# Optimization experiments

Hardware: AMD Instinct MI355X
Metric: run time of the kernel (lower is better)

The kernel has to match this reference:

```python
import jax, jax.numpy as jnp
from jax import lax
import numpy as np

B, T, F = 64, 128, 16
H = 512
S = 2  # num_seg; SEG_DICT['2'] = [8, 6], seg_cumsum = [2, 10, 16]


def timestep_embedding(t, dim, max_period=10000.0):
    half = dim // 2
    freqs = jnp.exp(-jnp.log(max_period) * jnp.arange(half, dtype=jnp.float32) / half)
    args = t[:, None] * freqs  # [N, half]
    return jnp.concatenate([jnp.cos(args), jnp.sin(args)], axis=-1)  # [N, dim]


def setup_inputs() -> dict:
    key = jax.random.key(0)
    ks = jax.random.split(key, 16)
    sc = lambda *sh: 1.0 / np.sqrt(sh[-1])
    inp = {
        'x': jax.random.normal(ks[0], (B, T, F), dtype=jnp.float32),
        'lengths': jax.random.randint(ks[1], (B,), 1, T + 1),
        'h0': jax.random.uniform(ks[2], (B, H), dtype=jnp.float32),
        'c0': jax.random.uniform(ks[3], (B, H), dtype=jnp.float32),
        'W_is0': jax.random.normal(ks[4], (H, 8), dtype=jnp.float32) * sc(8),
        'b_is0': jax.random.normal(ks[5], (H,), dtype=jnp.float32) * 0.01,
        'W_is1': jax.random.normal(ks[6], (H, 6), dtype=jnp.float32) * sc(6),
        'b_is1': jax.random.normal(ks[7], (H,), dtype=jnp.float32) * 0.01,
        'W_ih': jax.random.normal(ks[8], (4 * H, 3 * H), dtype=jnp.float32) * sc(3 * H),
        'W_hh': jax.random.normal(ks[9], (4 * H, H), dtype=jnp.float32) * sc(H),
        'b_ih': jax.random.normal(ks[10], (4 * H,), dtype=jnp.float32) * 0.01,
        'b_hh': jax.random.normal(ks[11], (4 * H,), dtype=jnp.float32) * 0.01,
        'W_o': jax.random.normal(ks[12], (F - 2, S * H), dtype=jnp.float32) * sc(S * H),
        'b_o': jax.random.normal(ks[13], (F - 2,), dtype=jnp.float32) * 0.01,
    }
    return inp


def reference(x, lengths, h0, c0, W_is0, b_is0, W_is1, b_is1,
              W_ih, W_hh, b_ih, b_hh, W_o, b_o):
    b, t, f = x.shape
    h = h0.shape[1]
    xf = x.reshape(-1, f)  # [B*T, F]

    # timestep embeddings from the two time columns (learning_type='diff')
    tc = timestep_embedding(xf[:, 0], h)
    tp = timestep_embedding(xf[:, 1], h)
    t_emb = jnp.concatenate([tc, tp], axis=-1)  # [B*T, 2H]

    # per-segment input linears (segments = cols 2:10 and 10:16)
    e0 = xf[:, 2:10] @ W_is0.T + b_is0
    e1 = xf[:, 10:16] @ W_is1.T + b_is1
    e0 = jnp.concatenate([e0, t_emb], axis=-1)[:, None, :]  # [B*T, 1, 3H]
    e1 = jnp.concatenate([e1, t_emb], axis=-1)[:, None, :]
    # faithful to torch: concat on dim=1 then reshape(batch, num_seg, seq_len, -1)
    embs = jnp.concatenate([e0, e1], axis=1).reshape(b, S, t, 3 * h)

    def cell(carry, xt):
        hh, cc = carry
        gates = xt @ W_ih.T + b_ih + hh @ W_hh.T + b_hh
        i, fg, g, o = jnp.split(gates, 4, axis=-1)  # torch LSTMCell order i,f,g,o
        cc = jax.nn.sigmoid(fg) * cc + jax.nn.sigmoid(i) * jnp.tanh(g)
        hh = jax.nn.sigmoid(o) * jnp.tanh(cc)
        return (hh, cc), hh

    hs = []
    for s in range(S):  # shared cell weights across segments (same nn.LSTMCell object)
        xs = jnp.swapaxes(embs[:, s], 0, 1)  # [T, B, 3H]
        _, h_seq = lax.scan(cell, (h0, c0), xs)  # [T, B, H]
        hs.append(jnp.swapaxes(h_seq, 0, 1))  # [B, T, H]
    hidden_states = jnp.stack(hs, axis=-2)  # [B, T, S, H]; dropout rate 0 -> identity

    idx = lengths - 1  # final valid timestep per sequence
    hfin = hidden_states[jnp.arange(b), idx].reshape(b, S * h)  # [B, S*H]
    out = jax.nn.sigmoid(hfin @ W_o.T + b_o)  # mlp_o: Linear + Sigmoid
    return out
```

## Files before the change

### kernel.cpp

```cpp
#include <hip/hip_runtime.h>
#include <hip/hip_bf16.h>
#include <stdint.h>


typedef __attribute__((ext_vector_type(8))) short bf16x8_t;
typedef __attribute__((ext_vector_type(4))) float f32x4_t;

#define SENT 0xAAAAAAAAu

#define OFF_G      0u
#define OFF_TEMB   33554432u
#define OFF_HH     50331648u
#define OFF_WHH    67239936u
#define OFF_WMID   69337088u
#define OFF_WC0    73531392u
#define OFF_WC1    73596928u
#define OFF_BC     73662464u
#define OFF_HFIN   73678848u

__device__ __forceinline__ float bf2f(uint16_t u){
  union { uint32_t i; float f; } v; v.i = ((uint32_t)u) << 16; return v.f;
}
__device__ __forceinline__ uint16_t f2b(float f){
  union { float f; uint32_t i; } v; v.f = f;
  uint32_t r = v.i + 0x7fffu + ((v.i >> 16) & 1u);
  return (uint16_t)(r >> 16);
}
__device__ __forceinline__ float sigm(float x){ return 1.0f/(1.0f + __expf(-x)); }
__device__ __forceinline__ float tanh_(float x){
  float xc = fminf(fmaxf(x, -15.f), 15.f);
  float t = __expf(2.f*xc);
  return (t - 1.f)/(t + 1.f);
}

__global__ void prep1(const float* __restrict__ W_ih, const float* __restrict__ W_hh,
                      const float* __restrict__ W_is0, const float* __restrict__ b_is0,
                      const float* __restrict__ W_is1, const float* __restrict__ b_is1,
                      const float* __restrict__ b_ih, const float* __restrict__ b_hh,
                      uint16_t* __restrict__ whh_b, uint16_t* __restrict__ wmid_b,
                      float* __restrict__ wc0, float* __restrict__ wc1, float* __restrict__ bc){
  const int n = blockIdx.x;
  const int tid = threadIdx.x;
  __shared__ float wrow[512];
  wrow[tid]       = W_ih[(size_t)n*1536 + tid];
  wrow[tid + 256] = W_ih[(size_t)n*1536 + 256 + tid];
  for (int j = tid; j < 1024; j += 256)
    wmid_b[(size_t)n*1024 + j] = f2b(W_ih[(size_t)n*1536 + 512 + j]);
  for (int k = tid; k < 512; k += 256)
    whh_b[(size_t)n*512 + k] = f2b(W_hh[(size_t)n*512 + k]);
  __syncthreads();
  if (tid < 8){
    float s = 0.f;
    for (int k = 0; k < 512; ++k) s += wrow[k]*W_is0[k*8 + tid];
    wc0[n*8 + tid] = s;
  } else if (tid < 16){
    int c = tid - 8;
    float s = 0.f;
    if (c < 6){ for (int k = 0; k < 512; ++k) s += wrow[k]*W_is1[k*6 + c]; }
    wc1[n*8 + c] = s;
  } else if (tid == 16){
    float s = b_ih[n] + b_hh[n];
    for (int k = 0; k < 512; ++k) s += wrow[k]*b_is0[k];
    bc[n] = s;
  } else if (tid == 17){
    float s = b_ih[n] + b_hh[n];
    for (int k = 0; k < 512; ++k) s += wrow[k]*b_is1[k];
    bc[2048 + n] = s;
  }
}

__global__ void prep2(const float* __restrict__ h0, uint16_t* __restrict__ h_hist){
  int i = blockIdx.x*256 + threadIdx.x;
  uint32_t* hh = (uint32_t*)h_hist;
  if (i < 32768){
    int rw = i >> 8, k = (i & 255)*2;
    uint32_t lo = f2b(h0[(size_t)(rw & 63)*512 + k]);
    uint32_t hi = f2b(h0[(size_t)(rw & 63)*512 + k + 1]);
    uint32_t w = lo | (hi << 16);
    if (w == SENT) w ^= 1u;
    hh[i] = w;
  } else if (i < 4227072){
    hh[i] = SENT;
  }
}

__global__ void tembk(const float* __restrict__ x, uint16_t* __restrict__ temb){
  const int rid = blockIdx.x;
  const int k = threadIdx.x;
  float x0 = x[(size_t)rid*16 + 0], x1 = x[(size_t)rid*16 + 1];
  float f = __expf((float)k * (-9.210340371976184f/256.f));
  float a0 = x0*f, a1 = x1*f;
  size_t base = (size_t)rid*1024;
  temb[base + k]        = f2b(__cosf(a0));
  temb[base + 256 + k]  = f2b(__sinf(a0));
  temb[base + 512 + k]  = f2b(__cosf(a1));
  temb[base + 768 + k]  = f2b(__sinf(a1));
}

__launch_bounds__(256)
__global__ void gemmB(const uint16_t* __restrict__ temb, const uint16_t* __restrict__ wmid,
                      uint16_t* __restrict__ G){
  __shared__ __align__(16) uint16_t Al[128][72];
  __shared__ __align__(16) uint16_t Bl[128][72];
  const int tid = threadIdx.x;
  const int m0 = blockIdx.x*128, n0 = blockIdx.y*128;
  const int w = tid >> 6, lane = tid & 63;
  const int q = lane >> 4, ln = lane & 15;
  const int wm = w >> 1, wn = w & 1;
  const int srow = tid >> 1, shalf = tid & 1;

  f32x4_t acc[4][4];
  #pragma unroll
  for (int a = 0; a < 4; ++a)
    #pragma unroll
    for (int b = 0; b < 4; ++b) acc[a][b] = (f32x4_t){0.f,0.f,0.f,0.f};

  for (int kb = 0; kb < 16; ++kb){
    const uint4* ga = (const uint4*)(temb + (size_t)(m0 + srow)*1024 + kb*64 + shalf*32);
    const uint4* gb = (const uint4*)(wmid + (size_t)(n0 + srow)*1024 + kb*64 + shalf*32);
    uint4 va[4], vb[4];
    #pragma unroll
    for (int i = 0; i < 4; ++i){ va[i] = ga[i]; vb[i] = gb[i]; }
    #pragma unroll
    for (int i = 0; i < 4; ++i){
      *(uint4*)&Al[srow][shalf*32 + i*8] = va[i];
      *(uint4*)&Bl[srow][shalf*32 + i*8] = vb[i];
    }
    __syncthreads();
    #pragma unroll
    for (int kc = 0; kc < 2; ++kc){
      bf16x8_t af[4], bf[4];
      #pragma unroll
      for (int mt = 0; mt < 4; ++mt) af[mt] = *(const bf16x8_t*)&Al[wm*64 + mt*16 + ln][kc*32 + q*8];
      #pragma unroll
      for (int nt = 0; nt < 4; ++nt) bf[nt] = *(const bf16x8_t*)&Bl[wn*64 + nt*16 + ln][kc*32 + q*8];
      #pragma unroll
      for (int mt = 0; mt < 4; ++mt)
        #pragma unroll
        for (int nt = 0; nt < 4; ++nt)
          acc[mt][nt] = __builtin_amdgcn_mfma_f32_16x16x32_bf16(af[mt], bf[nt], acc[mt][nt], 0, 0, 0);
    }
    __syncthreads();
  }
  #pragma unroll
  for (int mt = 0; mt < 4; ++mt)
    #pragma unroll
    for (int nt = 0; nt < 4; ++nt)
      #pragma unroll
      for (int r = 0; r < 4; ++r){
        int Mr = m0 + wm*64 + mt*16 + q*4 + r;
        int Nc = n0 + wn*64 + nt*16 + ln;
        G[(size_t)Mr*2048 + Nc] = f2b(acc[mt][nt][r]);
      }
}

__launch_bounds__(256)
__global__ void lstmk(const float* __restrict__ x, const float* __restrict__ c0,
                      const int* __restrict__ lengths,
                      const uint16_t* __restrict__ whh_b, const uint16_t* __restrict__ G,
                      const float* __restrict__ wc0, const float* __restrict__ wc1,
                      const float* __restrict__ bc,
                      uint16_t* __restrict__ h_hist, float* __restrict__ hfin){
  __shared__ __align__(16) uint16_t h_l[2][16][552];

  const int tid = threadIdx.x;
  const int bid = blockIdx.x;
  const int rr = bid & 7;
  const int g  = bid >> 3;
  const int k0 = g*32;
  const int sp = rr >> 2;
  const int w = tid >> 6, lane = tid & 63;
  const int q = lane >> 4, ln = lane & 15;
  const int u8 = ln & 7, gh = ln >> 3;
  const int unit = k0 + w*8 + u8;
  const int gl0 = gh*512 + unit;
  const int gl1 = (2 + gh)*512 + unit;

  bf16x8_t barr0[16], barr1[16];
  #pragma unroll
  for (int kc = 0; kc < 16; ++kc){
    barr0[kc] = *(const bf16x8_t*)(whh_b + (size_t)gl0*512 + kc*32 + q*8);
    barr1[kc] = *(const bf16x8_t*)(whh_b + (size_t)gl1*512 + kc*32 + q*8);
  }
  bf16x8_t e0f[2], e1f[2];
  #pragma unroll
  for (int nsI = 0; nsI < 2; ++nsI){
    bf16x8_t v0 = {0,0,0,0,0,0,0,0}, v1 = {0,0,0,0,0,0,0,0};
    if (q == 0){
      const float* wcs = nsI ? wc1 : wc0;
      #pragma unroll
      for (int j = 0; j < 8; ++j){
        ((uint16_t*)&v0)[j] = f2b(wcs[gl0*8 + j]);
        ((uint16_t*)&v1)[j] = f2b(wcs[gl1*8 + j]);
      }
    }
    e0f[nsI] = v0; e1f[nsI] = v1;
  }
  float bc0v[2] = { bc[gl0], bc[2048 + gl0] };
  float bc1v[2] = { bc[gl1], bc[2048 + gl1] };

  int   bmr[4], lenr[4];
  float cst[4];
  #pragma unroll
  for (int r = 0; r < 4; ++r){
    int row = rr*16 + q*4 + r;
    bmr[r]  = row & 63;
    lenr[r] = lengths[bmr[r]];
    cst[r]  = c0[(size_t)bmr[r]*512 + unit];
  }

  const int hm = tid >> 4, j = tid & 15;
  const int xm = tid >> 3, xc = tid & 7;
  const int xb = (rr*16 + xm) & 63;

  for (int idx = tid; idx < 2*16*32; idx += 256)
    h_l[idx >> 9][(idx >> 5) & 15][520 + (idx & 31)] = 0;

  for (int t = 0; t < 128; ++t){
    const int qidx = sp*128 + t;
    const int ntm = qidx >> 1;
    const int ns  = qidx & 1;

    uint16_t g0r[4], g1r[4];
    #pragma unroll
    for (int r = 0; r < 4; ++r){
      size_t grow = (size_t)(bmr[r]*128 + ntm)*2048;
      g0r[r] = G[grow + gl0];
      g1r[r] = G[grow + gl1];
    }
    float xv = 0.f;
    if (tid < 128){
      if (ns == 0)      xv = x[(size_t)(xb*128 + ntm)*16 + 2 + xc];
      else if (xc < 6)  xv = x[(size_t)(xb*128 + ntm)*16 + 10 + xc];
    }

    {
      unsigned long long* hp = (unsigned long long*)
          (h_hist + ((size_t)t*128 + rr*16 + hm)*512);
      unsigned long long hv[8];
      while (true){
        bool ok = true;
        #pragma unroll
        for (int i = 0; i < 8; ++i){
          hv[i] = __hip_atomic_load(&hp[j + 16*i], __ATOMIC_RELAXED, __HIP_MEMORY_SCOPE_AGENT);
          ok &= ((uint32_t)hv[i] != SENT) & ((uint32_t)(hv[i] >> 32) != SENT);
        }
        if (ok) break;
        __builtin_amdgcn_s_sleep(1);
      }
      #pragma unroll
      for (int i = 0; i < 8; ++i)
        *(unsigned long long*)&h_l[t & 1][hm][(j + 16*i)*4] = hv[i];
    }
    if (tid < 128) h_l[t & 1][xm][512 + xc] = f2b(xv);
    __syncthreads();

    f32x4_t acc0, acc1;
    {
      float b0 = ns ? bc0v[1] : bc0v[0];
      float b1 = ns ? bc1v[1] : bc1v[0];
      #pragma unroll
      for (int r = 0; r < 4; ++r){ acc0[r] = bf2f(g0r[r]) + b0; acc1[r] = bf2f(g1r[r]) + b1; }
    }
    #pragma unroll
    for (int kc = 0; kc < 16; ++kc){
      bf16x8_t a = *(const bf16x8_t*)&h_l[t & 1][ln][kc*32 + q*8];
      acc0 = __builtin_amdgcn_mfma_f32_16x16x32_bf16(a, barr0[kc], acc0, 0, 0, 0);
      acc1 = __builtin_amdgcn_mfma_f32_16x16x32_bf16(a, barr1[kc], acc1, 0, 0, 0);
    }
    {
      bf16x8_t a = *(const bf16x8_t*)&h_l[t & 1][ln][512 + q*8];
      acc0 = __builtin_amdgcn_mfma_f32_16x16x32_bf16(a, ns ? e0f[1] : e0f[0], acc0, 0, 0, 0);
      acc1 = __builtin_amdgcn_mfma_f32_16x16x32_bf16(a, ns ? e1f[1] : e1f[0], acc1, 0, 0, 0);
    }

    float pf[4], po[4];
    #pragma unroll
    for (int r = 0; r < 4; ++r){
      pf[r] = __shfl_xor(acc0[r], 8);
      po[r] = __shfl_xor(acc1[r], 8);
    }
    if (ln < 8){
      uint32_t hb[4]; float hF[4];
      #pragma unroll
      for (int r = 0; r < 4; ++r){
        float ig = acc0[r], fg = pf[r], gg = acc1[r], og = po[r];
        cst[r] = sigm(fg)*cst[r] + sigm(ig)*tanh_(gg);
        float h = sigm(og)*tanh_(cst[r]);
        hF[r] = h; hb[r] = (uint32_t)f2b(h);
      }
      #pragma unroll
      for (int r = 0; r < 4; ++r){
        uint32_t ph = (uint32_t)__shfl_xor((int)hb[r], 1);
        if (!(ln & 1)){
          uint32_t packed = hb[r] | (ph << 16);
          if (packed == SENT) packed ^= 1u;
          uint32_t* hp = (uint32_t*)(h_hist + ((size_t)(t+1)*128 + rr*16 + q*4 + r)*512 + unit);
          __hip_atomic_store(hp, packed, __ATOMIC_RELAXED, __HIP_MEMORY_SCOPE_AGENT);
        }
        if (t == lenr[r] - 1)
          hfin[(size_t)bmr[r]*1024 + sp*512 + unit] = hF[r];
      }
    }
  }
}

__global__ void outk(const float* __restrict__ hfin, const float* __restrict__ W_o,
                     const float* __restrict__ b_o, float* __restrict__ out){
  __shared__ float hl[1024];
  __shared__ float red[16][17];
  const int b = blockIdx.x, tid = threadIdx.x;
  #pragma unroll
  for (int i = 0; i < 4; ++i) hl[tid + i*256] = hfin[(size_t)b*1024 + tid + i*256];
  __syncthreads();
  const int o = tid >> 4, j0 = tid & 15;
  float s = 0.f;
  if (o < 14){
    for (int j = j0; j < 1024; j += 16) s += hl[j]*W_o[(size_t)o*1024 + j];
  }
  red[o][j0] = s;
  __syncthreads();
  if (tid < 14){
    float tot = b_o[tid];
    #pragma unroll
    for (int i = 0; i < 16; ++i) tot += red[tid][i];
    out[b*14 + tid] = 1.0f/(1.0f + __expf(-tot));
  }
}

extern "C" void kernel_launch(void* const* d_in, const int* in_sizes, int n_in,
                              void* d_out, int out_size, void* d_ws, size_t ws_size,
                              hipStream_t stream){
  const float* x     = (const float*)d_in[0];
  const int*   lens  = (const int*)  d_in[1];
  const float* h0    = (const float*)d_in[2];
  const float* c0    = (const float*)d_in[3];
  const float* W_is0 = (const float*)d_in[4];
  const float* b_is0 = (const float*)d_in[5];
  const float* W_is1 = (const float*)d_in[6];
  const float* b_is1 = (const float*)d_in[7];
  const float* W_ih  = (const float*)d_in[8];
  const float* W_hh  = (const float*)d_in[9];
  const float* b_ih  = (const float*)d_in[10];
  const float* b_hh  = (const float*)d_in[11];
  const float* W_o   = (const float*)d_in[12];
  const float* b_o   = (const float*)d_in[13];
  float* out = (float*)d_out;

  char* ws = (char*)d_ws;
  uint16_t* G      = (uint16_t*)(ws + OFF_G);
  uint16_t* temb   = (uint16_t*)(ws + OFF_TEMB);
  uint16_t* h_hist = (uint16_t*)(ws + OFF_HH);
  uint16_t* whh_b  = (uint16_t*)(ws + OFF_WHH);
  uint16_t* wmid_b = (uint16_t*)(ws + OFF_WMID);
  float* wc0  = (float*)(ws + OFF_WC0);
  float* wc1  = (float*)(ws + OFF_WC1);
  float* bc   = (float*)(ws + OFF_BC);
  float* hfin = (float*)(ws + OFF_HFIN);

  hipLaunchKernelGGL(prep1, dim3(2048), dim3(256), 0, stream,
                     W_ih, W_hh, W_is0, b_is0, W_is1, b_is1, b_ih, b_hh,
                     whh_b, wmid_b, wc0, wc1, bc);
  hipLaunchKernelGGL(prep2, dim3(16512), dim3(256), 0, stream, h0, h_hist);
  hipLaunchKernelGGL(tembk, dim3(8192), dim3(256), 0, stream, x, temb);
  hipLaunchKernelGGL(gemmB, dim3(64, 16), dim3(256), 0, stream, temb, wmid_b, G);
  hipLaunchKernelGGL(lstmk, dim3(128), dim3(256), 0, stream,
                     x, c0, lens, whh_b, G, wc0, wc1, bc, h_hist, hfin);
  hipLaunchKernelGGL(outk, dim3(64), dim3(256), 0, stream, hfin, W_o, b_o, out);
}
```

Before: 611.7 us.

## Halve LSTM grid, use 512-thread blocks, reuse own h slice locally

The recurrent LSTM kernel now runs on 64 blocks of 512 threads instead of 128 blocks of 256. Each block owns 64 hidden units and writes its new h slice straight into shared memory, so it only polls other blocks' slices in global memory. The h history layout is reorganised into per-block contiguous chunks, the spin wait uses a wave-wide __all check, and the MFMA accumulation is split into two independent chains to shorten dependency latency. Fewer blocks means fewer cross-block flag polls per step, but each block now does twice the work per step.

```diff
diff --git a/kernel.cpp b/kernel.cpp
--- a/kernel.cpp
+++ b/kernel.cpp
@@ -73,9 +73,16 @@
   int i = blockIdx.x*256 + threadIdx.x;
   uint32_t* hh = (uint32_t*)h_hist;
   if (i < 32768){
-    int rw = i >> 8, k = (i & 255)*2;
-    uint32_t lo = f2b(h0[(size_t)(rw & 63)*512 + k]);
-    uint32_t hi = f2b(h0[(size_t)(rw & 63)*512 + k + 1]);
+    int rr  = i >> 12;
+    int rem = i & 4095;
+    int cg  = rem >> 9;
+    int r2  = rem & 511;
+    int row = r2 >> 5;
+    int up  = (r2 & 31)*2;
+    int b    = (rr*16 + row) & 63;
+    int unit = cg*64 + up;
+    uint32_t lo = f2b(h0[(size_t)b*512 + unit]);
+    uint32_t hi = f2b(h0[(size_t)b*512 + unit + 1]);
     uint32_t w = lo | (hi << 16);
     if (w == SENT) w ^= 1u;
     hh[i] = w;
@@ -154,7 +161,7 @@
       }
 }
 
-__launch_bounds__(256)
+__launch_bounds__(512, 2)
 __global__ void lstmk(const float* __restrict__ x, const float* __restrict__ c0,
                       const int* __restrict__ lengths,
                       const uint16_t* __restrict__ whh_b, const uint16_t* __restrict__ G,
@@ -166,15 +173,16 @@
   const int tid = threadIdx.x;
   const int bid = blockIdx.x;
   const int rr = bid & 7;
-  const int g  = bid >> 3;
-  const int k0 = g*32;
+  const int cg = bid >> 3;
   const int sp = rr >> 2;
   const int w = tid >> 6, lane = tid & 63;
   const int q = lane >> 4, ln = lane & 15;
   const int u8 = ln & 7, gh = ln >> 3;
-  const int unit = k0 + w*8 + u8;
+  const int unit = cg*64 + w*8 + u8;
   const int gl0 = gh*512 + unit;
   const int gl1 = (2 + gh)*512 + unit;
+
+  const int LVL = 65536;
 
   bf16x8_t barr0[16], barr1[16];
   #pragma unroll
@@ -189,9 +197,9 @@
     if (q == 0){
       const float* wcs = nsI ? wc1 : wc0;
       #pragma unroll
-      for (int j = 0; j < 8; ++j){
-        ((uint16_t*)&v0)[j] = f2b(wcs[gl0*8 + j]);
-        ((uint16_t*)&v1)[j] = f2b(wcs[gl1*8 + j]);
+      for (int jj = 0; jj < 8; ++jj){
+        ((uint16_t*)&v0)[jj] = f2b(wcs[gl0*8 + jj]);
+        ((uint16_t*)&v1)[jj] = f2b(wcs[gl1*8 + jj]);
       }
     }
     e0f[nsI] = v0; e1f[nsI] = v1;
@@ -209,17 +217,34 @@
     cst[r]  = c0[(size_t)bmr[r]*512 + unit];
   }
 
-  const int hm = tid >> 4, j = tid & 15;
+  const int c1 = tid, c2 = tid + 512;
+  const int cgi1 = c1 >> 7, k1 = c1 & 127, prow1 = k1 >> 3, pcol1 = (k1 & 7)*8;
+  const int cgi2 = c2 >> 7, k2 = c2 & 127, prow2 = k2 >> 3, pcol2 = (k2 & 7)*8;
+  const bool skip1 = (cgi1 == cg), skip2 = (cgi2 == cg);
+  const size_t roff1 = (size_t)(rr*8 + cgi1)*1024 + prow1*64 + pcol1;
+  const size_t roff2 = (size_t)(rr*8 + cgi2)*1024 + prow2*64 + pcol2;
+
   const int xm = tid >> 3, xc = tid & 7;
   const int xb = (rr*16 + xm) & 63;
 
-  for (int idx = tid; idx < 2*16*32; idx += 256)
+  for (int idx = tid; idx < 2*16*32; idx += 512)
     h_l[idx >> 9][(idx >> 5) & 15][520 + (idx & 31)] = 0;
+
+  if (tid < 128){
+    int c = tid, kk = c & 127, pr = kk >> 3, pc = (kk & 7)*8;
+    const unsigned long long* hp = (const unsigned long long*)
+        (h_hist + (size_t)(rr*8 + cg)*1024 + pr*64 + pc);
+    unsigned long long a = __hip_atomic_load(&hp[0], __ATOMIC_RELAXED, __HIP_MEMORY_SCOPE_AGENT);
+    unsigned long long b = __hip_atomic_load(&hp[1], __ATOMIC_RELAXED, __HIP_MEMORY_SCOPE_AGENT);
+    *(unsigned long long*)&h_l[0][pr][cg*64 + pc]     = a;
+    *(unsigned long long*)&h_l[0][pr][cg*64 + pc + 4] = b;
+  }
 
   for (int t = 0; t < 128; ++t){
     const int qidx = sp*128 + t;
     const int ntm = qidx >> 1;
     const int ns  = qidx & 1;
+    const int buf = t & 1;
 
     uint16_t g0r[4], g1r[4];
     #pragma unroll
@@ -235,44 +260,67 @@
     }
 
     {
-      unsigned long long* hp = (unsigned long long*)
-          (h_hist + ((size_t)t*128 + rr*16 + hm)*512);
-      unsigned long long hv[8];
+      const unsigned long long* base = (const unsigned long long*)(h_hist + (size_t)t*LVL);
+      unsigned long long a1=0, b1=0, a2=0, b2=0;
+      const unsigned long long* p1 = base + (roff1 >> 2);
+      const unsigned long long* p2 = base + (roff2 >> 2);
       while (true){
         bool ok = true;
-        #pragma unroll
-        for (int i = 0; i < 8; ++i){
-          hv[i] = __hip_atomic_load(&hp[j + 16*i], __ATOMIC_RELAXED, __HIP_MEMORY_SCOPE_AGENT);
-          ok &= ((uint32_t)hv[i] != SENT) & ((uint32_t)(hv[i] >> 32) != SENT);
+        if (!skip1){
+          a1 = __hip_atomic_load(&p1[0], __ATOMIC_RELAXED, __HIP_MEMORY_SCOPE_AGENT);
+          b1 = __hip_atomic_load(&p1[1], __ATOMIC_RELAXED, __HIP_MEMORY_SCOPE_AGENT);
+          ok &= ((uint32_t)a1 != SENT) & ((uint32_t)(a1 >> 32) != SENT)
+              & ((uint32_t)b1 != SENT) & ((uint32_t)(b1 >> 32) != SENT);
         }
-        if (ok) break;
+        if (!skip2){
+          a2 = __hip_atomic_load(&p2[0], __ATOMIC_RELAXED, __HIP_MEMORY_SCOPE_AGENT);
+          b2 = __hip_atomic_load(&p2[1], __ATOMIC_RELAXED, __HIP_MEMORY_SCOPE_AGENT);
+          ok &= ((uint32_t)a2 != SENT) & ((uint32_t)(a2 >> 32) != SENT)
+              & ((uint32_t)b2 != SENT) & ((uint32_t)(b2 >> 32) != SENT);
+        }
+        if (__all(ok)) break;
         __builtin_amdgcn_s_sleep(1);
       }
-      #pragma unroll
-      for (int i = 0; i < 8; ++i)
-        *(unsigned long long*)&h_l[t & 1][hm][(j + 16*i)*4] = hv[i];
-    }
-    if (tid < 128) h_l[t & 1][xm][512 + xc] = f2b(xv);
+      if (!skip1){
+        *(unsigned long long*)&h_l[buf][prow1][cgi1*64 + pcol1]     = a1;
+        *(unsigned long long*)&h_l[buf][prow1][cgi1*64 + pcol1 + 4] = b1;
+      }
+      if (!skip2){
+        *(unsigned long long*)&h_l[buf][prow2][cgi2*64 + pcol2]     = a2;
+        *(unsigned long long*)&h_l[buf][prow2][cgi2*64 + pcol2 + 4] = b2;
+      }
+    }
+    if (tid < 128) h_l[buf][xm][512 + xc] = f2b(xv);
     __syncthreads();
 
-    f32x4_t acc0, acc1;
+    f32x4_t a0A, a1A;
+    f32x4_t a0B = (f32x4_t){0,0,0,0}, a1B = (f32x4_t){0,0,0,0};
     {
       float b0 = ns ? bc0v[1] : bc0v[0];
       float b1 = ns ? bc1v[1] : bc1v[0];
       #pragma unroll
-      for (int r = 0; r < 4; ++r){ acc0[r] = bf2f(g0r[r]) + b0; acc1[r] = bf2f(g1r[r]) + b1; }
-    }
-    #pragma unroll
-    for (int kc = 0; kc < 16; ++kc){
-      bf16x8_t a = *(const bf16x8_t*)&h_l[t & 1][ln][kc*32 + q*8];
-      acc0 = __builtin_amdgcn_mfma_f32_16x16x32_bf16(a, barr0[kc], acc0, 0, 0, 0);
-      acc1 = __builtin_amdgcn_mfma_f32_16x16x32_bf16(a, barr1[kc], acc1, 0, 0, 0);
+      for (int r = 0; r < 4; ++r){ a0A[r] = bf2f(g0r[r]) + b0; a1A[r] = bf2f(g1r[r]) + b1; }
+    }
+    #pragma unroll
+    for (int kc = 0; kc < 8; ++kc){
+      bf16x8_t a = *(const bf16x8_t*)&h_l[buf][ln][kc*32 + q*8];
+      a0A = __builtin_amdgcn_mfma_f32_16x16x32_bf16(a, barr0[kc], a0A, 0, 0, 0);
+      a1A = __builtin_amdgcn_mfma_f32_16x16x32_bf16(a, barr1[kc], a1A, 0, 0, 0);
+    }
+    #pragma unroll
+    for (int kc = 8; kc < 16; ++kc){
+      bf16x8_t a = *(const bf16x8_t*)&h_l[buf][ln][kc*32 + q*8];
+      a0B = __builtin_amdgcn_mfma_f32_16x16x32_bf16(a, barr0[kc], a0B, 0, 0, 0);
+      a1B = __builtin_amdgcn_mfma_f32_16x16x32_bf16(a, barr1[kc], a1B, 0, 0, 0);
     }
     {
-      bf16x8_t a = *(const bf16x8_t*)&h_l[t & 1][ln][512 + q*8];
-      acc0 = __builtin_amdgcn_mfma_f32_16x16x32_bf16(a, ns ? e0f[1] : e0f[0], acc0, 0, 0, 0);
-      acc1 = __builtin_amdgcn_mfma_f32_16x16x32_bf16(a, ns ? e1f[1] : e1f[0], acc1, 0, 0, 0);
-    }
+      bf16x8_t a = *(const bf16x8_t*)&h_l[buf][ln][512 + q*8];
+      a0B = __builtin_amdgcn_mfma_f32_16x16x32_bf16(a, ns ? e0f[1] : e0f[0], a0B, 0, 0, 0);
+      a1B = __builtin_amdgcn_mfma_f32_16x16x32_bf16(a, ns ? e1f[1] : e1f[0], a1B, 0, 0, 0);
+    }
+    f32x4_t acc0, acc1;
+    #pragma unroll
+    for (int r = 0; r < 4; ++r){ acc0[r] = a0A[r] + a0B[r]; acc1[r] = a1A[r] + a1B[r]; }
 
     float pf[4], po[4];
     #pragma unroll
@@ -295,7 +343,9 @@
         if (!(ln & 1)){
           uint32_t packed = hb[r] | (ph << 16);
           if (packed == SENT) packed ^= 1u;
-          uint32_t* hp = (uint32_t*)(h_hist + ((size_t)(t+1)*128 + rr*16 + q*4 + r)*512 + unit);
+          *(uint32_t*)&h_l[(t+1) & 1][q*4 + r][unit] = packed;
+          uint32_t* hp = (uint32_t*)(h_hist + (size_t)(t+1)*LVL
+                                     + (size_t)(rr*8 + cg)*1024 + (q*4 + r)*64 + w*8 + u8);
           __hip_atomic_store(hp, packed, __ATOMIC_RELAXED, __HIP_MEMORY_SCOPE_AGENT);
         }
         if (t == lenr[r] - 1)
@@ -364,7 +414,7 @@
   hipLaunchKernelGGL(prep2, dim3(16512), dim3(256), 0, stream, h0, h_hist);
   hipLaunchKernelGGL(tembk, dim3(8192), dim3(256), 0, stream, x, temb);
   hipLaunchKernelGGL(gemmB, dim3(64, 16), dim3(256), 0, stream, temb, wmid_b, G);
-  hipLaunchKernelGGL(lstmk, dim3(128), dim3(256), 0, stream,
+  hipLaunchKernelGGL(lstmk, dim3(64), dim3(512), 0, stream,
                      x, c0, lens, whh_b, G, wc0, wc1, bc, h_hist, hfin);
   hipLaunchKernelGGL(outk, dim3(64), dim3(256), 0, stream, hfin, W_o, b_o, out);
 }
```

Result: slower. 711.0 us (+16.2%).

## Reorganize h history into block-contiguous layout with wider 64-bit stores

Applied to the files above, without the earlier changes.

Changes the global h_hist layout so each producer block's 32 units for a 16-row group are stored contiguously, and packs four bf16 values per 64-bit atomic store instead of two per 32-bit store. Consumers poll with per-wave loads over contiguous 512-element chunks and use a wave-wide __all check. The prep kernel is updated to write h0 in the new layout. The aim is to cut the number of store transactions and make the polled loads more coalesced on the critical serial recurrence path, at the cost of more complex indexing.

```diff
diff --git a/kernel.cpp b/kernel.cpp
--- a/kernel.cpp
+++ b/kernel.cpp
@@ -73,12 +73,18 @@
   int i = blockIdx.x*256 + threadIdx.x;
   uint32_t* hh = (uint32_t*)h_hist;
   if (i < 32768){
-    int rw = i >> 8, k = (i & 255)*2;
-    uint32_t lo = f2b(h0[(size_t)(rw & 63)*512 + k]);
-    uint32_t hi = f2b(h0[(size_t)(rw & 63)*512 + k + 1]);
-    uint32_t w = lo | (hi << 16);
-    if (w == SENT) w ^= 1u;
-    hh[i] = w;
+    int e    = i*2;
+    int rrcg = e >> 9;
+    int rr   = rrcg >> 4, cg = rrcg & 15;
+    int rm   = e & 511;
+    int row  = rm >> 5, u = rm & 31;
+    int b    = (rr*16 + row) & 63;
+    int unit = cg*32 + u;
+    uint32_t lo = f2b(h0[(size_t)b*512 + unit]);
+    uint32_t hi = f2b(h0[(size_t)b*512 + unit + 1]);
+    uint32_t wd = lo | (hi << 16);
+    if (wd == SENT) wd ^= 1u;
+    hh[i] = wd;
   } else if (i < 4227072){
     hh[i] = SENT;
   }
@@ -176,6 +182,8 @@
   const int gl0 = gh*512 + unit;
   const int gl1 = (2 + gh)*512 + unit;
 
+  const int LVL = 65536;
+
   bf16x8_t barr0[16], barr1[16];
   #pragma unroll
   for (int kc = 0; kc < 16; ++kc){
@@ -189,9 +197,9 @@
     if (q == 0){
       const float* wcs = nsI ? wc1 : wc0;
       #pragma unroll
-      for (int j = 0; j < 8; ++j){
-        ((uint16_t*)&v0)[j] = f2b(wcs[gl0*8 + j]);
-        ((uint16_t*)&v1)[j] = f2b(wcs[gl1*8 + j]);
+      for (int jj = 0; jj < 8; ++jj){
+        ((uint16_t*)&v0)[jj] = f2b(wcs[gl0*8 + jj]);
+        ((uint16_t*)&v1)[jj] = f2b(wcs[gl1*8 + jj]);
       }
     }
     e0f[nsI] = v0; e1f[nsI] = v1;
@@ -209,9 +217,12 @@
     cst[r]  = c0[(size_t)bmr[r]*512 + unit];
   }
 
-  const int hm = tid >> 4, j = tid & 15;
+  const int prow = lane >> 2;
+  const int pcol = (lane & 3)*8;
   const int xm = tid >> 3, xc = tid & 7;
   const int xb = (rr*16 + xm) & 63;
+
+  const size_t stb = ((size_t)rr*8192 + g*512);
 
   for (int idx = tid; idx < 2*16*32; idx += 256)
     h_l[idx >> 9][(idx >> 5) & 15][520 + (idx & 31)] = 0;
@@ -220,6 +231,7 @@
     const int qidx = sp*128 + t;
     const int ntm = qidx >> 1;
     const int ns  = qidx & 1;
+    const int buf = t & 1;
 
     uint16_t g0r[4], g1r[4];
     #pragma unroll
@@ -235,24 +247,30 @@
     }
 
     {
-      unsigned long long* hp = (unsigned long long*)
-          (h_hist + ((size_t)t*128 + rr*16 + hm)*512);
-      unsigned long long hv[8];
+      const unsigned long long* lvl = (const unsigned long long*)h_hist
+                                      + (((size_t)t*LVL + (size_t)rr*8192) >> 2);
+      unsigned long long hv[4][2];
       while (true){
         bool ok = true;
         #pragma unroll
-        for (int i = 0; i < 8; ++i){
-          hv[i] = __hip_atomic_load(&hp[j + 16*i], __ATOMIC_RELAXED, __HIP_MEMORY_SCOPE_AGENT);
-          ok &= ((uint32_t)hv[i] != SENT) & ((uint32_t)(hv[i] >> 32) != SENT);
+        for (int i = 0; i < 4; ++i){
+          const unsigned long long* p = lvl + ((size_t)(w*4 + i)*128 + prow*8 + (pcol >> 2));
+          hv[i][0] = __hip_atomic_load(&p[0], __ATOMIC_RELAXED, __HIP_MEMORY_SCOPE_AGENT);
+          hv[i][1] = __hip_atomic_load(&p[1], __ATOMIC_RELAXED, __HIP_MEMORY_SCOPE_AGENT);
+          ok &= ((uint32_t)hv[i][0] != SENT) & ((uint32_t)(hv[i][0] >> 32) != SENT)
+              & ((uint32_t)hv[i][1] != SENT) & ((uint32_t)(hv[i][1] >> 32) != SENT);
         }
-        if (ok) break;
+        if (__all(ok)) break;
         __builtin_amdgcn_s_sleep(1);
       }
       #pragma unroll
-      for (int i = 0; i < 8; ++i)
-        *(unsigned long long*)&h_l[t & 1][hm][(j + 16*i)*4] = hv[i];
-    }
-    if (tid < 128) h_l[t & 1][xm][512 + xc] = f2b(xv);
+      for (int i = 0; i < 4; ++i){
+        int reg = w*4 + i;
+        *(unsigned long long*)&h_l[buf][prow][reg*32 + pcol]     = hv[i][0];
+        *(unsigned long long*)&h_l[buf][prow][reg*32 + pcol + 4] = hv[i][1];
+      }
+    }
+    if (tid < 128) h_l[buf][xm][512 + xc] = f2b(xv);
     __syncthreads();
 
     f32x4_t acc0, acc1;
@@ -264,12 +282,12 @@
     }
     #pragma unroll
     for (int kc = 0; kc < 16; ++kc){
-      bf16x8_t a = *(const bf16x8_t*)&h_l[t & 1][ln][kc*32 + q*8];
+      bf16x8_t a = *(const bf16x8_t*)&h_l[buf][ln][kc*32 + q*8];
       acc0 = __builtin_amdgcn_mfma_f32_16x16x32_bf16(a, barr0[kc], acc0, 0, 0, 0);
       acc1 = __builtin_amdgcn_mfma_f32_16x16x32_bf16(a, barr1[kc], acc1, 0, 0, 0);
     }
     {
-      bf16x8_t a = *(const bf16x8_t*)&h_l[t & 1][ln][512 + q*8];
+      bf16x8_t a = *(const bf16x8_t*)&h_l[buf][ln][512 + q*8];
       acc0 = __builtin_amdgcn_mfma_f32_16x16x32_bf16(a, ns ? e0f[1] : e0f[0], acc0, 0, 0, 0);
       acc1 = __builtin_amdgcn_mfma_f32_16x16x32_bf16(a, ns ? e1f[1] : e1f[0], acc1, 0, 0, 0);
     }
@@ -292,11 +310,14 @@
       #pragma unroll
       for (int r = 0; r < 4; ++r){
         uint32_t ph = (uint32_t)__shfl_xor((int)hb[r], 1);
-        if (!(ln & 1)){
-          uint32_t packed = hb[r] | (ph << 16);
-          if (packed == SENT) packed ^= 1u;
-          uint32_t* hp = (uint32_t*)(h_hist + ((size_t)(t+1)*128 + rr*16 + q*4 + r)*512 + unit);
-          __hip_atomic_store(hp, packed, __ATOMIC_RELAXED, __HIP_MEMORY_SCOPE_AGENT);
+        uint32_t packed = hb[r] | (ph << 16);
+        if (packed == SENT) packed ^= 1u;
+        uint32_t hi = (uint32_t)__shfl_xor((int)packed, 2);
+        if ((ln & 3) == 0){
+          unsigned long long v = (unsigned long long)packed | ((unsigned long long)hi << 32);
+          unsigned long long* hp = (unsigned long long*)h_hist
+              + (((size_t)(t+1)*LVL + stb + (size_t)(q*4 + r)*32 + w*8 + u8) >> 2);
+          __hip_atomic_store(hp, v, __ATOMIC_RELAXED, __HIP_MEMORY_SCOPE_AGENT);
         }
         if (t == lenr[r] - 1)
           hfin[(size_t)bmr[r]*1024 + sp*512 + unit] = hF[r];
```

New measurement: 600.0 us. About the same (-1.9%).
